# Optimization experiments

Measured on AMD Instinct MI355X. Metric: run time of the kernel, lower is better.

Reference implementation:

```python
import jax, jax.numpy as jnp
import numpy as np

B, N, D = 64, 1024, 1024

def setup_inputs() -> dict:
    key = jax.random.key(0)
    k1, k2, k3, k4, k5 = jax.random.split(key, 5)
    s = 1.0 / np.sqrt(D)
    return {
        "h_t": jax.random.normal(k1, (B, D), dtype=jnp.float32),
        "keys": jax.random.normal(k2, (B, N, D), dtype=jnp.float32),
        "W_h": jax.random.uniform(k3, (D, D), jnp.float32, -s, s),
        "W_k": jax.random.uniform(k4, (D, D), jnp.float32, -s, s),
        "v": jax.random.uniform(k5, (D,), jnp.float32, -s, s),
    }

def reference(h_t, keys, W_h, W_k, v):
    # W_h(h_t): [B, D]; W_k(keys): [B, N, D]  (nn.Linear computes x @ W.T)
    qh = h_t @ W_h.T                       # [B, D]
    kh = jnp.einsum('bnd,ed->bne', keys, W_k)  # [B, N, D]
    energy = jnp.tanh(qh[:, None, :] + kh)     # [B, N, D]
    scores = jnp.einsum('bnd,d->bn', energy, v)  # [B, N]
    alpha = jax.nn.softmax(scores, axis=-1)      # [B, N]
    context = jnp.einsum('bn,bnd->bd', alpha, keys)  # [B, D]
    return (context, alpha)
```

## Files before the change

kernel.cpp:

```cpp
#include <hip/hip_runtime.h>
#include <math.h>

#define BB 64
#define NN 1024
#define DD 1024

typedef __bf16 bf16x8 __attribute__((ext_vector_type(8)));
typedef _Float16 f16x8 __attribute__((ext_vector_type(8)));
typedef _Float16 f16x4 __attribute__((ext_vector_type(4)));
typedef float f32x4 __attribute__((ext_vector_type(4)));
typedef unsigned short u16x8 __attribute__((ext_vector_type(8)));

#define GLOAD_LDS16(g, l)                                                  \
    __builtin_amdgcn_global_load_lds(                                      \
        (const __attribute__((address_space(1))) unsigned int*)(g),        \
        (__attribute__((address_space(3))) unsigned int*)(l), 16, 0, 0)

__device__ __forceinline__ float fast_tanh(float x) {
    return 1.f - 2.f / (__expf(2.f * x) + 1.f);
}


__global__ __launch_bounds__(256) void cvt_all(const float* __restrict__ keys,
                                               const float* __restrict__ W_k,
                                               _Float16* __restrict__ keysT,
                                               _Float16* __restrict__ wkT) {
    const int nt = blockIdx.x;
    const int bb = blockIdx.y;
    const int t = threadIdx.x;
    const float* src = (bb == 64) ? (W_k + (size_t)nt * 128 * DD)
                                  : (keys + ((size_t)bb * NN + nt * 128) * DD);
    _Float16* dst = (bb == 64) ? (wkT + (size_t)nt * 32 * 4096)
                               : (keysT + (((size_t)bb * 8 + nt) * 32) * 4096);
    for (int kt = 0; kt < 32; ++kt) {
#pragma unroll
        for (int r = 0; r < 2; ++r) {
            const int p = r * 2048 + t * 8;
            const int n = p >> 5;
            const int k = p & 31;
            const float4* s4 = (const float4*)(src + (size_t)n * DD + kt * 32 + k);
            float4 a = s4[0], b4 = s4[1];
            f16x8 h = {(_Float16)a.x,  (_Float16)a.y,  (_Float16)a.z,  (_Float16)a.w,
                       (_Float16)b4.x, (_Float16)b4.y, (_Float16)b4.z, (_Float16)b4.w};
            *(f16x8*)(dst + (size_t)kt * 4096 + p) = h;
        }
    }
}

__global__ __launch_bounds__(256) void qh_fast(const float* __restrict__ h_t,
                                               const float* __restrict__ W_h,
                                               float* __restrict__ qh,
                                               float* __restrict__ scores) {
    __shared__ float hs[8 * 1024];
    __shared__ float red2[128][8];
    const int et = blockIdx.x;
    const int bg = blockIdx.y;
    const int t = threadIdx.x;
    const int bid = bg * 8 + et;
#pragma unroll
    for (int j = 0; j < 4; ++j) scores[bid * 1024 + j * 256 + t] = 0.f;
    const int b0 = bg * 8;
    const float4* hsrc = (const float4*)(h_t + (size_t)b0 * DD);
    float4* hdst = (float4*)hs;
    for (int i = t; i < 2048; i += 256) hdst[i] = hsrc[i];
    __syncthreads();
    const int el = t & 127;
    const int half = t >> 7;
    const int e = et * 128 + el;
    const float4* wrow = (const float4*)(W_h + (size_t)e * DD) + half * 128;
    float p[8];
#pragma unroll
    for (int bi = 0; bi < 8; ++bi) p[bi] = 0.f;
    for (int k4 = 0; k4 < 128; ++k4) {
        float4 wv = wrow[k4];
        const int kb = half * 512 + k4 * 4;
#pragma unroll
        for (int bi = 0; bi < 8; ++bi) {
            const float* hp = &hs[bi * 1024 + kb];
            p[bi] = fmaf(wv.x, hp[0], p[bi]);
            p[bi] = fmaf(wv.y, hp[1], p[bi]);
            p[bi] = fmaf(wv.z, hp[2], p[bi]);
            p[bi] = fmaf(wv.w, hp[3], p[bi]);
        }
    }
    if (half == 1) {
#pragma unroll
        for (int bi = 0; bi < 8; ++bi) red2[el][bi] = p[bi];
    }
    __syncthreads();
    if (half == 0) {
#pragma unroll
        for (int bi = 0; bi < 8; ++bi) qh[(size_t)(b0 + bi) * DD + e] = p[bi] + red2[el][bi];
    }
}

__global__ __launch_bounds__(256, 4) void scores_mfma(const _Float16* __restrict__ keysT,
                                                      const _Float16* __restrict__ wkT,
                                                      const float* __restrict__ v,
                                                      const float* __restrict__ qh,
                                                      float* __restrict__ scores) {
    __shared__ _Float16 As[2 * 128 * 32];
    __shared__ _Float16 Bs[2 * 128 * 32];
    __shared__ float vs[128];
    __shared__ float qs[128];
    __shared__ float red[128][2];

    const int tid = threadIdx.x;
    const int cp = blockIdx.x >> 3;
    const int nt = blockIdx.x & 7;
    const int b = blockIdx.y;
    const int e0 = cp * 128;

    if (tid < 128) {
        vs[tid] = v[e0 + tid];
        qs[tid] = qh[b * DD + e0 + tid];
    }

    const char* Abase = (const char*)(keysT + (((size_t)b * 8 + nt) * 32) * 4096);
    const char* Bbase = (const char*)(wkT + ((size_t)cp * 32) * 4096);

    const int w = tid >> 6;
    const int lane = tid & 63;
    const int wm = w & 1;
    const int we = w >> 1;
    const int lcol = lane & 15;
    const int quad = lane >> 4;
    const int soff = tid * 16;

    f32x4 acc[4][4];
#pragma unroll
    for (int mi = 0; mi < 4; ++mi)
#pragma unroll
        for (int ni = 0; ni < 4; ++ni) acc[mi][ni] = (f32x4){0.f, 0.f, 0.f, 0.f};

    for (int kt2 = 0; kt2 < 16; ++kt2) {
        __syncthreads();
        const char* ag = Abase + (size_t)kt2 * 16384 + soff;
        const char* bg = Bbase + (size_t)kt2 * 16384 + soff;
        char* al_ = (char*)As + soff;
        char* bl_ = (char*)Bs + soff;
#pragma unroll
        for (int r = 0; r < 4; ++r) GLOAD_LDS16(ag + r * 4096, al_ + r * 4096);
#pragma unroll
        for (int r = 0; r < 4; ++r) GLOAD_LDS16(bg + r * 4096, bl_ + r * 4096);
        __syncthreads();

#pragma unroll
        for (int c = 0; c < 2; ++c) {
            f16x8 af[4], bf[4];
#pragma unroll
            for (int mi = 0; mi < 4; ++mi)
                af[mi] = *(const f16x8*)&As[c * 4096 + (wm * 64 + mi * 16 + lcol) * 32 + quad * 8];
#pragma unroll
            for (int ni = 0; ni < 4; ++ni)
                bf[ni] = *(const f16x8*)&Bs[c * 4096 + (we * 64 + ni * 16 + lcol) * 32 + quad * 8];
#pragma unroll
            for (int mi = 0; mi < 4; ++mi)
#pragma unroll
                for (int ni = 0; ni < 4; ++ni)
                    acc[mi][ni] = __builtin_amdgcn_mfma_f32_16x16x32_f16(af[mi], bf[ni], acc[mi][ni], 0, 0, 0);
        }
    }

    float part[4][4];
#pragma unroll
    for (int mi = 0; mi < 4; ++mi)
#pragma unroll
        for (int r = 0; r < 4; ++r) part[mi][r] = 0.f;
#pragma unroll
    for (int mi = 0; mi < 4; ++mi)
#pragma unroll
        for (int ni = 0; ni < 4; ++ni) {
            const int e = we * 64 + ni * 16 + lcol;
            const float vv = vs[e];
            const float qv = qs[e];
#pragma unroll
            for (int r = 0; r < 4; ++r)
                part[mi][r] += vv * fast_tanh(qv + acc[mi][ni][r]);
        }
#pragma unroll
    for (int mi = 0; mi < 4; ++mi)
#pragma unroll
        for (int r = 0; r < 4; ++r) {
            float p = part[mi][r];
            p += __shfl_xor(p, 1);
            p += __shfl_xor(p, 2);
            p += __shfl_xor(p, 4);
            p += __shfl_xor(p, 8);
            if (lcol == 0) red[wm * 64 + mi * 16 + quad * 4 + r][we] = p;
        }
    __syncthreads();
    if (tid < 128) atomicAdd(&scores[b * NN + nt * 128 + tid], red[tid][0] + red[tid][1]);
}

__global__ __launch_bounds__(256) void softmax_kernel(const float* __restrict__ scores,
                                                      float* __restrict__ alpha,
                                                      float* __restrict__ context) {
    const int b = blockIdx.x;
    const int t = threadIdx.x;
#pragma unroll
    for (int j = 0; j < 4; ++j) context[b * DD + t + 256 * j] = 0.f;
    float x[4];
    float m = -1e30f;
#pragma unroll
    for (int j = 0; j < 4; ++j) {
        x[j] = scores[b * NN + t + 256 * j];
        m = fmaxf(m, x[j]);
    }
#pragma unroll
    for (int mask = 32; mask >= 1; mask >>= 1) m = fmaxf(m, __shfl_xor(m, mask));
    __shared__ float wred[4];
    __shared__ float wsum[4];
    const int wv = t >> 6;
    if ((t & 63) == 0) wred[wv] = m;
    __syncthreads();
    m = fmaxf(fmaxf(wred[0], wred[1]), fmaxf(wred[2], wred[3]));
    float s = 0.f;
#pragma unroll
    for (int j = 0; j < 4; ++j) {
        x[j] = expf(x[j] - m);
        s += x[j];
    }
#pragma unroll
    for (int mask = 32; mask >= 1; mask >>= 1) s += __shfl_xor(s, mask);
    if ((t & 63) == 0) wsum[wv] = s;
    __syncthreads();
    s = wsum[0] + wsum[1] + wsum[2] + wsum[3];
    const float inv = 1.f / s;
#pragma unroll
    for (int j = 0; j < 4; ++j) alpha[b * NN + t + 256 * j] = x[j] * inv;
}

__global__ __launch_bounds__(256) void context_f32(const float* __restrict__ keys,
                                                   const float* __restrict__ alpha,
                                                   float* __restrict__ context) {
    const int b = blockIdx.y;
    const int nc = blockIdx.x;
    const int t = threadIdx.x;
    __shared__ float al[64];
    if (t < 64) al[t] = alpha[b * NN + nc * 64 + t];
    __syncthreads();
    const float4* kp = (const float4*)(keys + ((size_t)b * NN + nc * 64) * DD);
    float4 acc = {0.f, 0.f, 0.f, 0.f};
#pragma unroll 4
    for (int n = 0; n < 64; ++n) {
        const float a = al[n];
        float4 kv = kp[(size_t)n * (DD / 4) + t];
        acc.x = fmaf(a, kv.x, acc.x);
        acc.y = fmaf(a, kv.y, acc.y);
        acc.z = fmaf(a, kv.z, acc.z);
        acc.w = fmaf(a, kv.w, acc.w);
    }
    float* cp = context + b * DD + 4 * t;
    atomicAdd(cp + 0, acc.x);
    atomicAdd(cp + 1, acc.y);
    atomicAdd(cp + 2, acc.z);
    atomicAdd(cp + 3, acc.w);
}

__global__ __launch_bounds__(256) void qh_fb(const float* __restrict__ h_t,
                                             const float* __restrict__ W_h,
                                             float* __restrict__ qh,
                                             float* __restrict__ scores) {
    __shared__ float hs[DD];
    const int b = blockIdx.y;
    const int e = blockIdx.x * 256 + threadIdx.x;
    scores[(blockIdx.y * 4 + blockIdx.x) * 256 + threadIdx.x] = 0.f;
    for (int i = threadIdx.x; i < DD; i += 256) hs[i] = h_t[b * DD + i];
    __syncthreads();
    const float4* wrow = (const float4*)(W_h + (size_t)e * DD);
    float acc = 0.f;
#pragma unroll 4
    for (int k4 = 0; k4 < DD / 4; ++k4) {
        float4 w = wrow[k4];
        acc = fmaf(w.x, hs[4 * k4 + 0], acc);
        acc = fmaf(w.y, hs[4 * k4 + 1], acc);
        acc = fmaf(w.z, hs[4 * k4 + 2], acc);
        acc = fmaf(w.w, hs[4 * k4 + 3], acc);
    }
    qh[b * DD + e] = acc;
}

#define SPAD 40
__device__ __forceinline__ void split16(const float4* __restrict__ src,
                                        unsigned short* hi, unsigned short* lo) {
    float x[16];
    float4 v0 = src[0], v1 = src[1], v2 = src[2], v3 = src[3];
    x[0] = v0.x; x[1] = v0.y; x[2] = v0.z; x[3] = v0.w;
    x[4] = v1.x; x[5] = v1.y; x[6] = v1.z; x[7] = v1.w;
    x[8] = v2.x; x[9] = v2.y; x[10] = v2.z; x[11] = v2.w;
    x[12] = v3.x; x[13] = v3.y; x[14] = v3.z; x[15] = v3.w;
#pragma unroll
    for (int i = 0; i < 16; ++i) {
        unsigned int u = __float_as_uint(x[i]);
        hi[i] = (unsigned short)(u >> 16);
        float hif = __uint_as_float(u & 0xFFFF0000u);
        float lof = x[i] - hif;
        lo[i] = (unsigned short)(__float_as_uint(lof) >> 16);
    }
}

__global__ __launch_bounds__(256, 2) void scores_fb(const float* __restrict__ keys,
                                                    const float* __restrict__ W_k,
                                                    const float* __restrict__ v,
                                                    const float* __restrict__ qh,
                                                    float* __restrict__ scores) {
    __shared__ unsigned short Ah[128 * SPAD];
    __shared__ unsigned short Al[128 * SPAD];
    __shared__ unsigned short Bh[128 * SPAD];
    __shared__ unsigned short Bl[128 * SPAD];
    __shared__ float vs[128];
    __shared__ float qs[128];
    __shared__ float red[128][2];

    const int tid = threadIdx.x;
    const int cp = blockIdx.x;
    const int rt = blockIdx.y;
    const int b = rt >> 3;
    const int n0 = (rt & 7) * 128;
    const int e0 = cp * 128;
    if (tid < 128) {
        vs[tid] = v[e0 + tid];
        qs[tid] = qh[b * DD + e0 + tid];
    }
    const float* Ag = keys + ((size_t)b * NN + n0) * DD;
    const float* Bg = W_k + (size_t)e0 * DD;
    const int w = tid >> 6;
    const int lane = tid & 63;
    const int wm = w & 1;
    const int we = w >> 1;
    const int lcol = lane & 15;
    const int quad = lane >> 4;
    f32x4 acc[4][4];
#pragma unroll
    for (int mi = 0; mi < 4; ++mi)
#pragma unroll
        for (int ni = 0; ni < 4; ++ni) acc[mi][ni] = (f32x4){0.f, 0.f, 0.f, 0.f};
    const int srow = tid >> 1;
    const int sseg = tid & 1;
    float4 pa[4], pb[4];
    {
        const float4* as = (const float4*)(Ag + (size_t)srow * DD + sseg * 16);
        const float4* bs = (const float4*)(Bg + (size_t)srow * DD + sseg * 16);
#pragma unroll
        for (int i = 0; i < 4; ++i) { pa[i] = as[i]; pb[i] = bs[i]; }
    }
    for (int kt = 0; kt < DD / 32; ++kt) {
        __syncthreads();
        {
            unsigned short hi[16], lo[16];
            split16(pa, hi, lo);
            u16x8* dh = (u16x8*)&Ah[srow * SPAD + sseg * 16];
            u16x8* dl = (u16x8*)&Al[srow * SPAD + sseg * 16];
            dh[0] = *(u16x8*)&hi[0]; dh[1] = *(u16x8*)&hi[8];
            dl[0] = *(u16x8*)&lo[0]; dl[1] = *(u16x8*)&lo[8];
            split16(pb, hi, lo);
            u16x8* eh = (u16x8*)&Bh[srow * SPAD + sseg * 16];
            u16x8* el = (u16x8*)&Bl[srow * SPAD + sseg * 16];
            eh[0] = *(u16x8*)&hi[0]; eh[1] = *(u16x8*)&hi[8];
            el[0] = *(u16x8*)&lo[0]; el[1] = *(u16x8*)&lo[8];
        }
        if (kt + 1 < DD / 32) {
            const int k0 = (kt + 1) * 32;
            const float4* as = (const float4*)(Ag + (size_t)srow * DD + k0 + sseg * 16);
            const float4* bs = (const float4*)(Bg + (size_t)srow * DD + k0 + sseg * 16);
#pragma unroll
            for (int i = 0; i < 4; ++i) { pa[i] = as[i]; pb[i] = bs[i]; }
        }
        __syncthreads();
        bf16x8 ah[4], al2[4], bh[4], bl2[4];
#pragma unroll
        for (int mi = 0; mi < 4; ++mi) {
            const int r = wm * 64 + mi * 16 + lcol;
            ah[mi] = *(const bf16x8*)&Ah[r * SPAD + quad * 8];
            al2[mi] = *(const bf16x8*)&Al[r * SPAD + quad * 8];
        }
#pragma unroll
        for (int ni = 0; ni < 4; ++ni) {
            const int r = we * 64 + ni * 16 + lcol;
            bh[ni] = *(const bf16x8*)&Bh[r * SPAD + quad * 8];
            bl2[ni] = *(const bf16x8*)&Bl[r * SPAD + quad * 8];
        }
#pragma unroll
        for (int mi = 0; mi < 4; ++mi)
#pragma unroll
            for (int ni = 0; ni < 4; ++ni) {
                acc[mi][ni] = __builtin_amdgcn_mfma_f32_16x16x32_bf16(ah[mi], bh[ni], acc[mi][ni], 0, 0, 0);
                acc[mi][ni] = __builtin_amdgcn_mfma_f32_16x16x32_bf16(ah[mi], bl2[ni], acc[mi][ni], 0, 0, 0);
                acc[mi][ni] = __builtin_amdgcn_mfma_f32_16x16x32_bf16(al2[mi], bh[ni], acc[mi][ni], 0, 0, 0);
            }
    }
    float part[4][4];
#pragma unroll
    for (int mi = 0; mi < 4; ++mi)
#pragma unroll
        for (int r = 0; r < 4; ++r) part[mi][r] = 0.f;
#pragma unroll
    for (int mi = 0; mi < 4; ++mi)
#pragma unroll
        for (int ni = 0; ni < 4; ++ni) {
            const int e = we * 64 + ni * 16 + lcol;
            const float vv = vs[e];
            const float qv = qs[e];
#pragma unroll
            for (int r = 0; r < 4; ++r)
                part[mi][r] += vv * fast_tanh(qv + acc[mi][ni][r]);
        }
#pragma unroll
    for (int mi = 0; mi < 4; ++mi)
#pragma unroll
        for (int r = 0; r < 4; ++r) {
            float p = part[mi][r];
            p += __shfl_xor(p, 1);
            p += __shfl_xor(p, 2);
            p += __shfl_xor(p, 4);
            p += __shfl_xor(p, 8);
            if (lcol == 0) red[wm * 64 + mi * 16 + quad * 4 + r][we] = p;
        }
    __syncthreads();
    if (tid < 128) atomicAdd(&scores[b * NN + n0 + tid], red[tid][0] + red[tid][1]);
}

extern "C" void kernel_launch(void* const* d_in, const int* in_sizes, int n_in,
                              void* d_out, int out_size, void* d_ws, size_t ws_size,
                              hipStream_t stream) {
    const float* h_t = (const float*)d_in[0];
    const float* keys = (const float*)d_in[1];
    const float* W_h = (const float*)d_in[2];
    const float* W_k = (const float*)d_in[3];
    const float* v = (const float*)d_in[4];

    float* context = (float*)d_out;
    float* alpha = (float*)d_out + BB * DD;
    float* qh = (float*)d_ws;
    float* scores = (float*)d_ws + BB * DD;

    const size_t wkT_off = (size_t)2 * BB * DD * sizeof(float);
    const size_t keysT_off = wkT_off + (size_t)DD * DD * 2;
    const size_t need = keysT_off + (size_t)BB * NN * DD * 2;

    if (ws_size >= need) {
        _Float16* wkT = (_Float16*)((char*)d_ws + wkT_off);
        _Float16* keysT = (_Float16*)((char*)d_ws + keysT_off);
        cvt_all<<<dim3(8, 65), 256, 0, stream>>>(keys, W_k, keysT, wkT);
        qh_fast<<<dim3(8, 8), 256, 0, stream>>>(h_t, W_h, qh, scores);
        scores_mfma<<<dim3(64, 64), 256, 0, stream>>>(keysT, wkT, v, qh, scores);
        softmax_kernel<<<BB, 256, 0, stream>>>(scores, alpha, context);
        context_f32<<<dim3(16, BB), 256, 0, stream>>>(keys, alpha, context);
    } else {
        qh_fb<<<dim3(4, BB), 256, 0, stream>>>(h_t, W_h, qh, scores);
        scores_fb<<<dim3(8, 512), 256, 0, stream>>>(keys, W_k, v, qh, scores);
        softmax_kernel<<<BB, 256, 0, stream>>>(scores, alpha, context);
        context_f32<<<dim3(16, BB), 256, 0, stream>>>(keys, alpha, context);
    }
}
```

Baseline: 646.6 us.

## Compute context from fp16 transposed keys and split conversion and qh grids

The context kernel now reads the already-converted fp16 keysT buffer instead of fp32 keys. It reduces over N inside a block per (batch, k-tile), which removes the atomics and the context zeroing. The conversion kernel is split along K into four grid slices for more parallelism. The qh kernel moves to one block per batch row with more blocks. The fp16 context reduces accuracy, and the qh change re-reads W_h per batch.

```diff
diff --git a/kernel.cpp b/kernel.cpp
--- a/kernel.cpp
+++ b/kernel.cpp
@@ -7,7 +7,6 @@
 
 typedef __bf16 bf16x8 __attribute__((ext_vector_type(8)));
 typedef _Float16 f16x8 __attribute__((ext_vector_type(8)));
-typedef _Float16 f16x4 __attribute__((ext_vector_type(4)));
 typedef float f32x4 __attribute__((ext_vector_type(4)));
 typedef unsigned short u16x8 __attribute__((ext_vector_type(8)));
 
@@ -21,84 +20,70 @@
 }
 
 
-__global__ __launch_bounds__(256) void cvt_all(const float* __restrict__ keys,
-                                               const float* __restrict__ W_k,
-                                               _Float16* __restrict__ keysT,
-                                               _Float16* __restrict__ wkT) {
+__global__ __launch_bounds__(256) void k_cvt(const float* __restrict__ keys,
+                                             const float* __restrict__ W_k,
+                                             _Float16* __restrict__ keysT,
+                                             _Float16* __restrict__ wkT) {
     const int nt = blockIdx.x;
     const int bb = blockIdx.y;
+    const int ks = blockIdx.z;
     const int t = threadIdx.x;
     const float* src = (bb == 64) ? (W_k + (size_t)nt * 128 * DD)
                                   : (keys + ((size_t)bb * NN + nt * 128) * DD);
     _Float16* dst = (bb == 64) ? (wkT + (size_t)nt * 32 * 4096)
                                : (keysT + (((size_t)bb * 8 + nt) * 32) * 4096);
-    for (int kt = 0; kt < 32; ++kt) {
+    const int p0 = t * 8;
+    const int n0 = p0 >> 5;
+    const int k0 = p0 & 31;
+    for (int kt = ks * 8; kt < ks * 8 + 8; ++kt) {
 #pragma unroll
         for (int r = 0; r < 2; ++r) {
-            const int p = r * 2048 + t * 8;
-            const int n = p >> 5;
-            const int k = p & 31;
-            const float4* s4 = (const float4*)(src + (size_t)n * DD + kt * 32 + k);
+            const int n = n0 + r * 64;
+            const float4* s4 = (const float4*)(src + (size_t)n * DD + kt * 32 + k0);
             float4 a = s4[0], b4 = s4[1];
             f16x8 h = {(_Float16)a.x,  (_Float16)a.y,  (_Float16)a.z,  (_Float16)a.w,
                        (_Float16)b4.x, (_Float16)b4.y, (_Float16)b4.z, (_Float16)b4.w};
-            *(f16x8*)(dst + (size_t)kt * 4096 + p) = h;
-        }
-    }
-}
-
-__global__ __launch_bounds__(256) void qh_fast(const float* __restrict__ h_t,
-                                               const float* __restrict__ W_h,
-                                               float* __restrict__ qh,
-                                               float* __restrict__ scores) {
-    __shared__ float hs[8 * 1024];
-    __shared__ float red2[128][8];
-    const int et = blockIdx.x;
-    const int bg = blockIdx.y;
+            *(f16x8*)(dst + (size_t)kt * 4096 + r * 2048 + p0) = h;
+        }
+    }
+}
+
+__global__ __launch_bounds__(256) void k_qh(const float* __restrict__ h_t,
+                                            const float* __restrict__ W_h,
+                                            float* __restrict__ qh,
+                                            float* __restrict__ scores) {
+    __shared__ float hs[DD];
+    __shared__ float red2[128];
+    const int b = blockIdx.x;
+    const int et = blockIdx.y;
     const int t = threadIdx.x;
-    const int bid = bg * 8 + et;
-#pragma unroll
-    for (int j = 0; j < 4; ++j) scores[bid * 1024 + j * 256 + t] = 0.f;
-    const int b0 = bg * 8;
-    const float4* hsrc = (const float4*)(h_t + (size_t)b0 * DD);
-    float4* hdst = (float4*)hs;
-    for (int i = t; i < 2048; i += 256) hdst[i] = hsrc[i];
+    if (t < 128) scores[b * NN + et * 128 + t] = 0.f;
+    ((float4*)hs)[t] = ((const float4*)(h_t + (size_t)b * DD))[t];
     __syncthreads();
     const int el = t & 127;
     const int half = t >> 7;
     const int e = et * 128 + el;
     const float4* wrow = (const float4*)(W_h + (size_t)e * DD) + half * 128;
-    float p[8];
-#pragma unroll
-    for (int bi = 0; bi < 8; ++bi) p[bi] = 0.f;
+    const float* hp = hs + half * 512;
+    float acc = 0.f;
+#pragma unroll 4
     for (int k4 = 0; k4 < 128; ++k4) {
         float4 wv = wrow[k4];
-        const int kb = half * 512 + k4 * 4;
-#pragma unroll
-        for (int bi = 0; bi < 8; ++bi) {
-            const float* hp = &hs[bi * 1024 + kb];
-            p[bi] = fmaf(wv.x, hp[0], p[bi]);
-            p[bi] = fmaf(wv.y, hp[1], p[bi]);
-            p[bi] = fmaf(wv.z, hp[2], p[bi]);
-            p[bi] = fmaf(wv.w, hp[3], p[bi]);
-        }
-    }
-    if (half == 1) {
-#pragma unroll
-        for (int bi = 0; bi < 8; ++bi) red2[el][bi] = p[bi];
-    }
-    __syncthreads();
-    if (half == 0) {
-#pragma unroll
-        for (int bi = 0; bi < 8; ++bi) qh[(size_t)(b0 + bi) * DD + e] = p[bi] + red2[el][bi];
-    }
-}
-
-__global__ __launch_bounds__(256, 4) void scores_mfma(const _Float16* __restrict__ keysT,
-                                                      const _Float16* __restrict__ wkT,
-                                                      const float* __restrict__ v,
-                                                      const float* __restrict__ qh,
-                                                      float* __restrict__ scores) {
+        acc = fmaf(wv.x, hp[4 * k4 + 0], acc);
+        acc = fmaf(wv.y, hp[4 * k4 + 1], acc);
+        acc = fmaf(wv.z, hp[4 * k4 + 2], acc);
+        acc = fmaf(wv.w, hp[4 * k4 + 3], acc);
+    }
+    if (half == 1) red2[el] = acc;
+    __syncthreads();
+    if (half == 0) qh[(size_t)b * DD + e] = acc + red2[el];
+}
+
+__global__ __launch_bounds__(256, 4) void k_sc(const _Float16* __restrict__ keysT,
+                                               const _Float16* __restrict__ wkT,
+                                               const float* __restrict__ v,
+                                               const float* __restrict__ qh,
+                                               float* __restrict__ scores) {
     __shared__ _Float16 As[2 * 128 * 32];
     __shared__ _Float16 Bs[2 * 128 * 32];
     __shared__ float vs[128];
@@ -193,13 +178,10 @@
     if (tid < 128) atomicAdd(&scores[b * NN + nt * 128 + tid], red[tid][0] + red[tid][1]);
 }
 
-__global__ __launch_bounds__(256) void softmax_kernel(const float* __restrict__ scores,
-                                                      float* __restrict__ alpha,
-                                                      float* __restrict__ context) {
+__global__ __launch_bounds__(256) void k_sm(const float* __restrict__ scores,
+                                            float* __restrict__ alpha) {
     const int b = blockIdx.x;
     const int t = threadIdx.x;
-#pragma unroll
-    for (int j = 0; j < 4; ++j) context[b * DD + t + 256 * j] = 0.f;
     float x[4];
     float m = -1e30f;
 #pragma unroll
@@ -231,31 +213,44 @@
     for (int j = 0; j < 4; ++j) alpha[b * NN + t + 256 * j] = x[j] * inv;
 }
 
-__global__ __launch_bounds__(256) void context_f32(const float* __restrict__ keys,
-                                                   const float* __restrict__ alpha,
-                                                   float* __restrict__ context) {
+__global__ __launch_bounds__(256) void k_ctx(const _Float16* __restrict__ keysT,
+                                             const float* __restrict__ alpha,
+                                             float* __restrict__ context) {
+    __shared__ float al[NN];
+    __shared__ float red[64][33];
+    const int kt = blockIdx.x;
     const int b = blockIdx.y;
-    const int nc = blockIdx.x;
     const int t = threadIdx.x;
-    __shared__ float al[64];
-    if (t < 64) al[t] = alpha[b * NN + nc * 64 + t];
-    __syncthreads();
-    const float4* kp = (const float4*)(keys + ((size_t)b * NN + nc * 64) * DD);
-    float4 acc = {0.f, 0.f, 0.f, 0.f};
-#pragma unroll 4
-    for (int n = 0; n < 64; ++n) {
-        const float a = al[n];
-        float4 kv = kp[(size_t)n * (DD / 4) + t];
-        acc.x = fmaf(a, kv.x, acc.x);
-        acc.y = fmaf(a, kv.y, acc.y);
-        acc.z = fmaf(a, kv.z, acc.z);
-        acc.w = fmaf(a, kv.w, acc.w);
-    }
-    float* cp = context + b * DD + 4 * t;
-    atomicAdd(cp + 0, acc.x);
-    atomicAdd(cp + 1, acc.y);
-    atomicAdd(cp + 2, acc.z);
-    atomicAdd(cp + 3, acc.w);
+#pragma unroll
+    for (int j = 0; j < 4; ++j) al[t + 256 * j] = alpha[b * NN + t + 256 * j];
+    __syncthreads();
+
+    const int p0 = t * 8;
+    const int g = t >> 2;
+    const int q = t & 3;
+    float acc[8];
+#pragma unroll
+    for (int j = 0; j < 8; ++j) acc[j] = 0.f;
+
+    for (int nt = 0; nt < 8; ++nt) {
+        const _Float16* base = keysT + (((size_t)b * 8 + nt) * 32 + kt) * 4096;
+#pragma unroll
+        for (int r = 0; r < 2; ++r) {
+            f16x8 kv = *(const f16x8*)(base + r * 2048 + p0);
+            const float a = al[nt * 128 + r * 64 + g];
+#pragma unroll
+            for (int j = 0; j < 8; ++j) acc[j] = fmaf(a, (float)kv[j], acc[j]);
+        }
+    }
+#pragma unroll
+    for (int j = 0; j < 8; ++j) red[g][q * 8 + j] = acc[j];
+    __syncthreads();
+    if (t < 32) {
+        float s = 0.f;
+#pragma unroll 8
+        for (int n = 0; n < 64; ++n) s += red[n][t];
+        context[(size_t)b * DD + kt * 32 + t] = s;
+    }
 }
 
 __global__ __launch_bounds__(256) void qh_fb(const float* __restrict__ h_t,
@@ -421,6 +416,71 @@
     if (tid < 128) atomicAdd(&scores[b * NN + n0 + tid], red[tid][0] + red[tid][1]);
 }
 
+__global__ __launch_bounds__(256) void sm_fb(const float* __restrict__ scores,
+                                             float* __restrict__ alpha,
+                                             float* __restrict__ context) {
+    const int b = blockIdx.x;
+    const int t = threadIdx.x;
+#pragma unroll
+    for (int j = 0; j < 4; ++j) context[b * DD + t + 256 * j] = 0.f;
+    float x[4];
+    float m = -1e30f;
+#pragma unroll
+    for (int j = 0; j < 4; ++j) {
+        x[j] = scores[b * NN + t + 256 * j];
+        m = fmaxf(m, x[j]);
+    }
+#pragma unroll
+    for (int mask = 32; mask >= 1; mask >>= 1) m = fmaxf(m, __shfl_xor(m, mask));
+    __shared__ float wred[4];
+    __shared__ float wsum[4];
+    const int wv = t >> 6;
+    if ((t & 63) == 0) wred[wv] = m;
+    __syncthreads();
+    m = fmaxf(fmaxf(wred[0], wred[1]), fmaxf(wred[2], wred[3]));
+    float s = 0.f;
+#pragma unroll
+    for (int j = 0; j < 4; ++j) {
+        x[j] = expf(x[j] - m);
+        s += x[j];
+    }
+#pragma unroll
+    for (int mask = 32; mask >= 1; mask >>= 1) s += __shfl_xor(s, mask);
+    if ((t & 63) == 0) wsum[wv] = s;
+    __syncthreads();
+    s = wsum[0] + wsum[1] + wsum[2] + wsum[3];
+    const float inv = 1.f / s;
+#pragma unroll
+    for (int j = 0; j < 4; ++j) alpha[b * NN + t + 256 * j] = x[j] * inv;
+}
+
+__global__ __launch_bounds__(256) void ctx_fb(const float* __restrict__ keys,
+                                              const float* __restrict__ alpha,
+                                              float* __restrict__ context) {
+    const int b = blockIdx.y;
+    const int nc = blockIdx.x;
+    const int t = threadIdx.x;
+    __shared__ float al[64];
+    if (t < 64) al[t] = alpha[b * NN + nc * 64 + t];
+    __syncthreads();
+    const float4* kp = (const float4*)(keys + ((size_t)b * NN + nc * 64) * DD);
+    float4 acc = {0.f, 0.f, 0.f, 0.f};
+#pragma unroll 4
+    for (int n = 0; n < 64; ++n) {
+        const float a = al[n];
+        float4 kv = kp[(size_t)n * (DD / 4) + t];
+        acc.x = fmaf(a, kv.x, acc.x);
+        acc.y = fmaf(a, kv.y, acc.y);
+        acc.z = fmaf(a, kv.z, acc.z);
+        acc.w = fmaf(a, kv.w, acc.w);
+    }
+    float* cp = context + b * DD + 4 * t;
+    atomicAdd(cp + 0, acc.x);
+    atomicAdd(cp + 1, acc.y);
+    atomicAdd(cp + 2, acc.z);
+    atomicAdd(cp + 3, acc.w);
+}
+
 extern "C" void kernel_launch(void* const* d_in, const int* in_sizes, int n_in,
                               void* d_out, int out_size, void* d_ws, size_t ws_size,
                               hipStream_t stream) {
@@ -442,15 +502,15 @@
     if (ws_size >= need) {
         _Float16* wkT = (_Float16*)((char*)d_ws + wkT_off);
         _Float16* keysT = (_Float16*)((char*)d_ws + keysT_off);
-        cvt_all<<<dim3(8, 65), 256, 0, stream>>>(keys, W_k, keysT, wkT);
-        qh_fast<<<dim3(8, 8), 256, 0, stream>>>(h_t, W_h, qh, scores);
-        scores_mfma<<<dim3(64, 64), 256, 0, stream>>>(keysT, wkT, v, qh, scores);
-        softmax_kernel<<<BB, 256, 0, stream>>>(scores, alpha, context);
-        context_f32<<<dim3(16, BB), 256, 0, stream>>>(keys, alpha, context);
+        k_cvt<<<dim3(8, 65, 4), 256, 0, stream>>>(keys, W_k, keysT, wkT);
+        k_qh<<<dim3(64, 8), 256, 0, stream>>>(h_t, W_h, qh, scores);
+        k_sc<<<dim3(64, 64), 256, 0, stream>>>(keysT, wkT, v, qh, scores);
+        k_sm<<<BB, 256, 0, stream>>>(scores, alpha);
+        k_ctx<<<dim3(32, 64), 256, 0, stream>>>(keysT, alpha, context);
     } else {
         qh_fb<<<dim3(4, BB), 256, 0, stream>>>(h_t, W_h, qh, scores);
         scores_fb<<<dim3(8, 512), 256, 0, stream>>>(keys, W_k, v, qh, scores);
-        softmax_kernel<<<BB, 256, 0, stream>>>(scores, alpha, context);
-        context_f32<<<dim3(16, BB), 256, 0, stream>>>(keys, alpha, context);
-    }
-}
+        sm_fb<<<BB, 256, 0, stream>>>(scores, alpha, context);
+        ctx_fb<<<dim3(16, BB), 256, 0, stream>>>(keys, alpha, context);
+    }
+}
```

After: 623.0 us. -3.7%, faster.
